# Optimization experiments

Hardware: AMD Instinct MI355X
Metric: run time of the kernel (lower is better)

The kernel has to match this reference:

```python
import jax, jax.numpy as jnp
import numpy as np

B, T, D, U = 32, 2048, 1024, 1024


def setup_inputs() -> dict:
    key = jax.random.key(0)
    ks = jax.random.split(key, 6)
    scale = 0.02
    return {
        "query": jax.random.normal(ks[0], (B, D), jnp.float32),
        "values": jax.random.normal(ks[1], (B, T, D), jnp.float32),
        "W1_k": jax.random.normal(ks[2], (D, U), jnp.float32) * scale,
        "W1_b": jnp.zeros((U,), jnp.float32),
        "W2_k": jax.random.normal(ks[3], (D, U), jnp.float32) * scale,
        "W2_b": jnp.zeros((U,), jnp.float32),
        "V_k": jax.random.normal(ks[4], (U, 1), jnp.float32) * scale,
        "V_b": jnp.zeros((1,), jnp.float32),
    }


def reference(query, values, W1_k, W1_b, W2_k, W2_b, V_k, V_b):
    # query: [B, D] -> [B, 1, U]; values: [B, T, D] -> [B, T, U]
    q_proj = (query @ W1_k + W1_b)[:, None, :]
    v_proj = jnp.einsum("btd,du->btu", values, W2_k) + W2_b
    # score: [B, T, 1]
    score = jnp.tanh(q_proj + v_proj) @ V_k + V_b
    attention_weights = jax.nn.softmax(score, axis=1)  # over time axis T
    context_vector = jnp.sum(attention_weights * values, axis=1)  # [B, D]
    return context_vector
```

## Files before the change

kernel.cpp:

```cpp
#include <hip/hip_runtime.h>

#define NB 32
#define NT 2048
#define ND 1024
#define NU 1024
#define NM (NB*NT)

using f32x4 = __attribute__((ext_vector_type(4))) float;
using s16x8 = __attribute__((ext_vector_type(8))) short;

#define BAR()    asm volatile("s_barrier" ::: "memory")
#define LGKM0()  asm volatile("s_waitcnt lgkmcnt(0)" ::: "memory")
#define VMC(n)   asm volatile("s_waitcnt vmcnt(" #n ")" ::: "memory")
#define SB0()    __builtin_amdgcn_sched_barrier(0)
#define P1()     __builtin_amdgcn_s_setprio(1)
#define P0()     __builtin_amdgcn_s_setprio(0)

__device__ __forceinline__ unsigned short f2bf(float f) {
  unsigned u = __builtin_bit_cast(unsigned, f);
  u = u + 0x7fffu + ((u >> 16) & 1u);
  return (unsigned short)(u >> 16);
}

__device__ __forceinline__ void gload_lds16(const void* g, void* l) {
  __builtin_amdgcn_global_load_lds(
      (const __attribute__((address_space(1))) unsigned int*)g,
      (__attribute__((address_space(3))) unsigned int*)l, 16, 0, 0);
}

__device__ __forceinline__ float tanh_fast(float x) {
  float e = __expf(2.0f * x);
  return 1.0f - 2.0f * __builtin_amdgcn_rcpf(e + 1.0f);
}

__device__ __forceinline__ void stage_half(const unsigned short* g, int kt, int h,
                                           unsigned short* lds, int w, int r3, int c8s) {
#pragma unroll
  for (int i = 0; i < 2; ++i) {
    int cb = i * 8 + w;
    gload_lds16(g + ((size_t)(h * 128 + cb * 8 + r3) << 10) + kt * 64 + c8s * 8,
                lds + h * 8192 + cb * 512);
  }
}

#define RD_FA(base, m0) \
  _Pragma("unroll") for (int m_ = 0; m_ < 4; ++m_) { \
    _Pragma("unroll") for (int ks_ = 0; ks_ < 2; ++ks_) { \
      int row_ = wr * 128 + ((m0) + m_) * 16 + l15; \
      int c_ = (ks_ * 4 + lg) ^ (row_ & 7); \
      fa[m_][ks_] = *(const s16x8*)((base) + row_ * 64 + c_ * 8); } }

#define RD_FB(dst, base, n0) \
  _Pragma("unroll") for (int n_ = 0; n_ < 2; ++n_) { \
    _Pragma("unroll") for (int ks_ = 0; ks_ < 2; ++ks_) { \
      int row_ = wc * 64 + ((n0) + n_) * 16 + l15; \
      int c_ = (ks_ * 4 + lg) ^ (row_ & 7); \
      (dst)[n_][ks_] = *(const s16x8*)((base) + row_ * 64 + c_ * 8); } }

#define MF(mb, fbx, nb) \
  _Pragma("unroll") for (int m_ = 0; m_ < 4; ++m_) \
    _Pragma("unroll") for (int n_ = 0; n_ < 2; ++n_) \
      _Pragma("unroll") for (int ks_ = 0; ks_ < 2; ++ks_) \
        acc[(mb) + m_][(nb) + n_] = __builtin_amdgcn_mfma_f32_16x16x32_bf16( \
            fa[m_][ks_], (fbx)[n_][ks_], acc[(mb) + m_][(nb) + n_], 0, 0, 0);

template<bool TAIL>
__device__ __forceinline__ void iter8(
    int i, const unsigned short* gA, const unsigned short* gB,
    unsigned short* sA, unsigned short* sB, f32x4 (&acc)[8][4],
    int w, int r3, int c8s, int wr, int wc, int l15, int lg) {
  const unsigned short* d0A = sA;
  const unsigned short* d0B = sB;
  const unsigned short* d1A = sA + 16384;
  const unsigned short* d1B = sB + 16384;
  s16x8 fa[4][2], fbA[2][2], fbB[2][2];
  const int kt0 = 2 * i;
  RD_FA(d0A, 0); RD_FB(fbA, d0B, 0);
  stage_half(gA, kt0 + 1, 1, sA + 16384, w, r3, c8s);
  BAR(); LGKM0(); SB0();
  P1(); MF(0, fbA, 0); P0();
  BAR();
  RD_FB(fbB, d0B, 2);
  stage_half(gB, kt0 + 1, 0, sB + 16384, w, r3, c8s);
  BAR(); LGKM0(); SB0();
  P1(); MF(0, fbB, 2); P0();
  BAR();
  RD_FA(d0A, 4);
  stage_half(gB, kt0 + 1, 1, sB + 16384, w, r3, c8s);
  BAR(); LGKM0(); SB0();
  P1(); MF(4, fbB, 2); P0();
  BAR();
  if (!TAIL) { stage_half(gA, kt0 + 2, 0, sA, w, r3, c8s); VMC(2); }
  else { VMC(0); }
  BAR(); SB0();
  P1(); MF(4, fbA, 0); P0();
  BAR();
  RD_FA(d1A, 0); RD_FB(fbA, d1B, 0);
  if (!TAIL) stage_half(gA, kt0 + 2, 1, sA, w, r3, c8s);
  BAR(); LGKM0(); SB0();
  P1(); MF(0, fbA, 0); P0();
  BAR();
  RD_FB(fbB, d1B, 2);
  if (!TAIL) stage_half(gB, kt0 + 2, 0, sB, w, r3, c8s);
  BAR(); LGKM0(); SB0();
  P1(); MF(0, fbB, 2); P0();
  BAR();
  RD_FA(d1A, 4);
  if (!TAIL) stage_half(gB, kt0 + 2, 1, sB, w, r3, c8s);
  BAR(); LGKM0(); SB0();
  P1(); MF(4, fbB, 2); P0();
  BAR();
  if (!TAIL) { stage_half(gA, kt0 + 3, 0, sA + 16384, w, r3, c8s); VMC(2); }
  BAR(); SB0();
  P1(); MF(4, fbA, 0); P0();
  BAR();
}

__global__ __launch_bounds__(512, 2) void k_score_gemm8(
    const unsigned short* __restrict__ vbf, const unsigned short* __restrict__ W2t,
    const float* __restrict__ add2, const float* __restrict__ Vk,
    float* __restrict__ score_part) {
  __shared__ unsigned short sA[32768];
  __shared__ unsigned short sB[32768];
  const int tid = threadIdx.x;
  const int w = tid >> 6;
  const int lane = tid & 63;
  const int wr = w >> 2, wc = w & 3;
  const int l15 = lane & 15, lg = lane >> 4;
  const int r3 = lane >> 3, c8s = (lane & 7) ^ r3;

  const int L = blockIdx.x;
  const int g = (L & 7) * 128 + (L >> 3);
  const int mtile = g >> 2, ntile = g & 3;

  const unsigned short* gA = vbf + ((size_t)mtile << 18);
  const unsigned short* gB = W2t + ((size_t)ntile << 18);

  f32x4 acc[8][4] = {};

  stage_half(gA, 0, 0, sA, w, r3, c8s);
  stage_half(gA, 0, 1, sA, w, r3, c8s);
  stage_half(gB, 0, 0, sB, w, r3, c8s);
  stage_half(gB, 0, 1, sB, w, r3, c8s);
  stage_half(gA, 1, 0, sA + 16384, w, r3, c8s);
  VMC(2);
  BAR();

#pragma unroll 1
  for (int i = 0; i < 7; ++i)
    iter8<false>(i, gA, gB, sA, sB, acc, w, r3, c8s, wr, wc, l15, lg);
  iter8<true>(7, gA, gB, sA, sB, acc, w, r3, c8s, wr, wc, l15, lg);

  const int b = (mtile * 256) >> 11;
  float vks[4], adds[4];
#pragma unroll
  for (int n = 0; n < 4; ++n) {
    int u = ntile * 256 + wc * 64 + n * 16 + l15;
    vks[n] = Vk[u];
    adds[n] = add2[(b << 10) + u];
  }
  __syncthreads();
  float* part = (float*)sA;
#pragma unroll
  for (int m = 0; m < 8; ++m) {
#pragma unroll
    for (int j = 0; j < 4; ++j) {
      float s = 0.f;
#pragma unroll
      for (int n = 0; n < 4; ++n) {
        float x = acc[m][n][j] + adds[n];
        s = fmaf(tanh_fast(x), vks[n], s);
      }
#pragma unroll
      for (int off = 1; off < 16; off <<= 1) s += __shfl_xor(s, off);
      if (l15 == 0) part[wc * 256 + wr * 128 + m * 16 + lg * 4 + j] = s;
    }
  }
  __syncthreads();
  if (tid < 256) {
    float v = part[tid] + part[256 + tid] + part[512 + tid] + part[768 + tid];
    score_part[((size_t)ntile << 16) + mtile * 256 + tid] = v;
  }
}

__global__ void k_qproj(const float* __restrict__ q, const float* __restrict__ W1,
                        const float* __restrict__ W1b, const float* __restrict__ W2b,
                        float* __restrict__ add2) {
  int u = blockIdx.x * 256 + threadIdx.x;
  int b = blockIdx.y;
  const float* qr = q + (b << 10);
  float s = 0.f;
#pragma unroll 8
  for (int d = 0; d < ND; ++d) s = fmaf(qr[d], W1[d * NU + u], s);
  add2[(b << 10) + u] = s + W1b[u] + W2b[u];
}

__global__ void k_w2t(const float* __restrict__ W2, unsigned short* __restrict__ W2t) {
  __shared__ unsigned short tile[64][65];
  int bu = blockIdx.x * 64, bd = blockIdx.y * 64;
  int x = threadIdx.x & 63, y4 = threadIdx.x >> 6;
#pragma unroll
  for (int r = 0; r < 16; ++r) {
    int dl = y4 * 16 + r;
    tile[x][dl] = f2bf(W2[(size_t)(bd + dl) * NU + bu + x]);
  }
  __syncthreads();
#pragma unroll
  for (int r = 0; r < 16; ++r) {
    int ul = y4 * 16 + r;
    W2t[(size_t)(bu + ul) * ND + bd + x] = tile[ul][x];
  }
}

__global__ void k_cvt_values(const float4* __restrict__ v, ushort4* __restrict__ o) {
  const int n4 = NM * ND / 4;
  for (int i = blockIdx.x * blockDim.x + threadIdx.x; i < n4; i += gridDim.x * blockDim.x) {
    float4 f = v[i];
    ushort4 h;
    h.x = f2bf(f.x); h.y = f2bf(f.y); h.z = f2bf(f.z); h.w = f2bf(f.w);
    o[i] = h;
  }
}

__global__ void k_softmax(const float* __restrict__ sp, float* __restrict__ w) {
  __shared__ float redm[4], reds[4];
  int b = blockIdx.x, tid = threadIdx.x;
  float s[8];
  float mx = -1e30f;
#pragma unroll
  for (int i = 0; i < 8; ++i) {
    int t = i * 256 + tid;
    float v = 0.f;
#pragma unroll
    for (int p = 0; p < 4; ++p) v += sp[((size_t)p << 16) + (b << 11) + t];
    s[i] = v;
    mx = fmaxf(mx, v);
  }
#pragma unroll
  for (int o = 1; o < 64; o <<= 1) mx = fmaxf(mx, __shfl_xor(mx, o));
  if ((tid & 63) == 0) redm[tid >> 6] = mx;
  __syncthreads();
  mx = fmaxf(fmaxf(redm[0], redm[1]), fmaxf(redm[2], redm[3]));
  float sum = 0.f;
#pragma unroll
  for (int i = 0; i < 8; ++i) { s[i] = __expf(s[i] - mx); sum += s[i]; }
#pragma unroll
  for (int o = 1; o < 64; o <<= 1) sum += __shfl_xor(sum, o);
  if ((tid & 63) == 0) reds[tid >> 6] = sum;
  __syncthreads();
  float inv = 1.0f / (reds[0] + reds[1] + reds[2] + reds[3]);
#pragma unroll
  for (int i = 0; i < 8; ++i) w[(b << 11) + i * 256 + tid] = s[i] * inv;
}

__global__ void k_context(const float* __restrict__ values, const float* __restrict__ wv,
                          float* __restrict__ part) {
  int d4 = threadIdx.x;
  int b = blockIdx.y, tc = blockIdx.z;
  const float4* vb = (const float4*)(values + ((size_t)b << 21) + ((size_t)tc << 17)) + d4;
  const float* wb = wv + (b << 11) + (tc << 7);
  float ax = 0.f, ay = 0.f, az = 0.f, aw = 0.f;
#pragma unroll 4
  for (int t = 0; t < 128; ++t) {
    float4 v = vb[(size_t)t << 8];
    float wt = wb[t];
    ax = fmaf(wt, v.x, ax); ay = fmaf(wt, v.y, ay);
    az = fmaf(wt, v.z, az); aw = fmaf(wt, v.w, aw);
  }
  float4* po = (float4*)(part + (((size_t)tc * NB + b) << 10)) + d4;
  *po = make_float4(ax, ay, az, aw);
}

__global__ void k_ctx_reduce(const float* __restrict__ part, float* __restrict__ out) {
  int i = blockIdx.x * 256 + threadIdx.x;
  float s = 0.f;
#pragma unroll
  for (int p = 0; p < 16; ++p) s += part[(p << 15) + i];
  out[i] = s;
}

extern "C" void kernel_launch(void* const* d_in, const int* in_sizes, int n_in,
                              void* d_out, int out_size, void* d_ws, size_t ws_size,
                              hipStream_t stream) {
  const float* query  = (const float*)d_in[0];
  const float* values = (const float*)d_in[1];
  const float* W1k    = (const float*)d_in[2];
  const float* W1b    = (const float*)d_in[3];
  const float* W2k    = (const float*)d_in[4];
  const float* W2b    = (const float*)d_in[5];
  const float* Vk     = (const float*)d_in[6];
  float* out = (float*)d_out;
  char* ws = (char*)d_ws;

  size_t off = 0;
  float* add2 = (float*)(ws + off); off += (size_t)NB * NU * 4;
  float* sp   = (float*)(ws + off); off += (size_t)4 * NM * 4;
  float* wv   = (float*)(ws + off); off += (size_t)NM * 4;
  float* ctxp = (float*)(ws + off); off += (size_t)16 * NB * ND * 4;
  unsigned short* W2t = (unsigned short*)(ws + off); off += (size_t)NU * ND * 2;
  unsigned short* vbf = (unsigned short*)(ws + off); off += (size_t)NM * ND * 2;

  k_qproj<<<dim3(4, 32), 256, 0, stream>>>(query, W1k, W1b, W2b, add2);
  k_w2t<<<dim3(16, 16), 256, 0, stream>>>(W2k, W2t);
  k_cvt_values<<<dim3(2048), 256, 0, stream>>>((const float4*)values, (ushort4*)vbf);
  k_score_gemm8<<<dim3(1024), 512, 0, stream>>>(vbf, W2t, add2, Vk, sp);
  k_softmax<<<dim3(32), 256, 0, stream>>>(sp, wv);
  k_context<<<dim3(1, 32, 16), 256, 0, stream>>>(values, wv, ctxp);
  k_ctx_reduce<<<dim3(128), 256, 0, stream>>>(ctxp, out);
}
```

Before: 343.6 us.

## Software-pipeline LDS fragment reads across MFMA phases with partial lgkm waits

Restructures the double-buffered GEMM inner loop so LDS fragment reads for the next phase are issued before the current MFMA batch. Partial lgkmcnt waits replace full drains, and the A fragments are split into two persistent register sets carried across iterations. Global-to-LDS staging is regrouped, with the whole next k-tile prefetched in the prologue, and several barriers are removed. This aims to hide LDS latency behind matrix math at the cost of more VGPRs, which may reduce occupancy or spill, and it makes synchronisation correctness more delicate.

```diff
diff --git a/kernel.cpp b/kernel.cpp
--- a/kernel.cpp
+++ b/kernel.cpp
@@ -10,7 +10,7 @@
 using s16x8 = __attribute__((ext_vector_type(8))) short;
 
 #define BAR()    asm volatile("s_barrier" ::: "memory")
-#define LGKM0()  asm volatile("s_waitcnt lgkmcnt(0)" ::: "memory")
+#define LGKMC(n) asm volatile("s_waitcnt lgkmcnt(" #n ")" ::: "memory")
 #define VMC(n)   asm volatile("s_waitcnt vmcnt(" #n ")" ::: "memory")
 #define SB0()    __builtin_amdgcn_sched_barrier(0)
 #define P1()     __builtin_amdgcn_s_setprio(1)
@@ -43,76 +43,79 @@
   }
 }
 
-#define RD_FA(base, m0) \
+#define RD_FA2(dst, base, m0) \
   _Pragma("unroll") for (int m_ = 0; m_ < 4; ++m_) { \
     _Pragma("unroll") for (int ks_ = 0; ks_ < 2; ++ks_) { \
       int row_ = wr * 128 + ((m0) + m_) * 16 + l15; \
       int c_ = (ks_ * 4 + lg) ^ (row_ & 7); \
-      fa[m_][ks_] = *(const s16x8*)((base) + row_ * 64 + c_ * 8); } }
-
-#define RD_FB(dst, base, n0) \
+      (dst)[m_][ks_] = *(const s16x8*)((base) + row_ * 64 + c_ * 8); } }
+
+#define RD_FB2(dst, base, n0) \
   _Pragma("unroll") for (int n_ = 0; n_ < 2; ++n_) { \
     _Pragma("unroll") for (int ks_ = 0; ks_ < 2; ++ks_) { \
       int row_ = wc * 64 + ((n0) + n_) * 16 + l15; \
       int c_ = (ks_ * 4 + lg) ^ (row_ & 7); \
       (dst)[n_][ks_] = *(const s16x8*)((base) + row_ * 64 + c_ * 8); } }
 
-#define MF(mb, fbx, nb) \
+#define MFQ(fax, mb, fbx, nb) \
   _Pragma("unroll") for (int m_ = 0; m_ < 4; ++m_) \
     _Pragma("unroll") for (int n_ = 0; n_ < 2; ++n_) \
       _Pragma("unroll") for (int ks_ = 0; ks_ < 2; ++ks_) \
         acc[(mb) + m_][(nb) + n_] = __builtin_amdgcn_mfma_f32_16x16x32_bf16( \
-            fa[m_][ks_], (fbx)[n_][ks_], acc[(mb) + m_][(nb) + n_], 0, 0, 0);
+            (fax)[m_][ks_], (fbx)[n_][ks_], acc[(mb) + m_][(nb) + n_], 0, 0, 0);
 
 template<bool TAIL>
 __device__ __forceinline__ void iter8(
     int i, const unsigned short* gA, const unsigned short* gB,
     unsigned short* sA, unsigned short* sB, f32x4 (&acc)[8][4],
+    s16x8 (&fa03)[4][2], s16x8 (&fa47)[4][2], s16x8 (&fbA)[2][2], s16x8 (&fbB)[2][2],
     int w, int r3, int c8s, int wr, int wc, int l15, int lg) {
   const unsigned short* d0A = sA;
   const unsigned short* d0B = sB;
   const unsigned short* d1A = sA + 16384;
   const unsigned short* d1B = sB + 16384;
-  s16x8 fa[4][2], fbA[2][2], fbB[2][2];
   const int kt0 = 2 * i;
-  RD_FA(d0A, 0); RD_FB(fbA, d0B, 0);
-  stage_half(gA, kt0 + 1, 1, sA + 16384, w, r3, c8s);
-  BAR(); LGKM0(); SB0();
-  P1(); MF(0, fbA, 0); P0();
-  BAR();
-  RD_FB(fbB, d0B, 2);
-  stage_half(gB, kt0 + 1, 0, sB + 16384, w, r3, c8s);
-  BAR(); LGKM0(); SB0();
-  P1(); MF(0, fbB, 2); P0();
-  BAR();
-  RD_FA(d0A, 4);
-  stage_half(gB, kt0 + 1, 1, sB + 16384, w, r3, c8s);
-  BAR(); LGKM0(); SB0();
-  P1(); MF(4, fbB, 2); P0();
-  BAR();
-  if (!TAIL) { stage_half(gA, kt0 + 2, 0, sA, w, r3, c8s); VMC(2); }
-  else { VMC(0); }
-  BAR(); SB0();
-  P1(); MF(4, fbA, 0); P0();
-  BAR();
-  RD_FA(d1A, 0); RD_FB(fbA, d1B, 0);
+  RD_FB2(fbB, d0B, 2);
+  LGKMC(4); SB0();
+  P1(); MFQ(fa03, 0, fbA, 0); P0();
+  BAR();
+  RD_FA2(fa47, d0A, 4);
+  LGKMC(8); SB0();
+  P1(); MFQ(fa03, 0, fbB, 2); P0();
+  BAR();
+  LGKMC(0); SB0();
+  P1(); MFQ(fa47, 4, fbB, 2); P0();
+  VMC(0);
+  BAR();
+  if (!TAIL) stage_half(gA, kt0 + 2, 0, sA, w, r3, c8s);
+  RD_FA2(fa03, d1A, 0);
+  SB0();
+  P1(); MFQ(fa47, 4, fbA, 0); P0();
+  RD_FB2(fbA, d1B, 0);
+  BAR();
   if (!TAIL) stage_half(gA, kt0 + 2, 1, sA, w, r3, c8s);
-  BAR(); LGKM0(); SB0();
-  P1(); MF(0, fbA, 0); P0();
-  BAR();
-  RD_FB(fbB, d1B, 2);
-  if (!TAIL) stage_half(gB, kt0 + 2, 0, sB, w, r3, c8s);
-  BAR(); LGKM0(); SB0();
-  P1(); MF(0, fbB, 2); P0();
-  BAR();
-  RD_FA(d1A, 4);
-  if (!TAIL) stage_half(gB, kt0 + 2, 1, sB, w, r3, c8s);
-  BAR(); LGKM0(); SB0();
-  P1(); MF(4, fbB, 2); P0();
-  BAR();
-  if (!TAIL) { stage_half(gA, kt0 + 3, 0, sA + 16384, w, r3, c8s); VMC(2); }
-  BAR(); SB0();
-  P1(); MF(4, fbA, 0); P0();
+  RD_FB2(fbB, d1B, 2);
+  LGKMC(4); SB0();
+  P1(); MFQ(fa03, 0, fbA, 0); P0();
+  BAR();
+  if (!TAIL) { stage_half(gB, kt0 + 2, 0, sB, w, r3, c8s);
+               stage_half(gB, kt0 + 2, 1, sB, w, r3, c8s); }
+  RD_FA2(fa47, d1A, 4);
+  LGKMC(8); SB0();
+  P1(); MFQ(fa03, 0, fbB, 2); P0();
+  BAR();
+  if (!TAIL) { stage_half(gB, kt0 + 3, 0, sB + 16384, w, r3, c8s);
+               stage_half(gB, kt0 + 3, 1, sB + 16384, w, r3, c8s); }
+  LGKMC(0); SB0();
+  P1(); MFQ(fa47, 4, fbB, 2); P0();
+  if (!TAIL) { VMC(4); }
+  BAR();
+  if (!TAIL) { stage_half(gA, kt0 + 3, 0, sA + 16384, w, r3, c8s);
+               stage_half(gA, kt0 + 3, 1, sA + 16384, w, r3, c8s);
+               RD_FA2(fa03, d0A, 0); }
+  SB0();
+  P1(); MFQ(fa47, 4, fbA, 0); P0();
+  if (!TAIL) RD_FB2(fbA, d0B, 0);
   BAR();
 }
 
@@ -137,19 +140,25 @@
   const unsigned short* gB = W2t + ((size_t)ntile << 18);
 
   f32x4 acc[8][4] = {};
+  s16x8 fa03[4][2], fa47[4][2], fbA[2][2], fbB[2][2];
 
   stage_half(gA, 0, 0, sA, w, r3, c8s);
   stage_half(gA, 0, 1, sA, w, r3, c8s);
   stage_half(gB, 0, 0, sB, w, r3, c8s);
   stage_half(gB, 0, 1, sB, w, r3, c8s);
+  stage_half(gB, 1, 0, sB + 16384, w, r3, c8s);
+  stage_half(gB, 1, 1, sB + 16384, w, r3, c8s);
   stage_half(gA, 1, 0, sA + 16384, w, r3, c8s);
-  VMC(2);
-  BAR();
+  stage_half(gA, 1, 1, sA + 16384, w, r3, c8s);
+  VMC(8);
+  BAR();
+  RD_FA2(fa03, sA, 0);
+  RD_FB2(fbA, sB, 0);
 
 #pragma unroll 1
   for (int i = 0; i < 7; ++i)
-    iter8<false>(i, gA, gB, sA, sB, acc, w, r3, c8s, wr, wc, l15, lg);
-  iter8<true>(7, gA, gB, sA, sB, acc, w, r3, c8s, wr, wc, l15, lg);
+    iter8<false>(i, gA, gB, sA, sB, acc, fa03, fa47, fbA, fbB, w, r3, c8s, wr, wc, l15, lg);
+  iter8<true>(7, gA, gB, sA, sB, acc, fa03, fa47, fbA, fbB, w, r3, c8s, wr, wc, l15, lg);
 
   const int b = (mtile * 256) >> 11;
   float vks[4], adds[4];
```

After: 439.8 us. +28.0%, slower.
